# Kernel optimization log

Hardware: AMD Instinct MI355X
Metric: run time of the kernel (lower is better)

The kernel has to match this reference:

```python
import jax, jax.numpy as jnp
import numpy as np

N_VERT = 163842  # icosphere level-7 vertex count
IN_FEATS = 64
OUT_FEATS = 64
BATCH = 2
K = 7  # center vertex + 6 one-ring neighbors


def setup_inputs() -> dict:
    key = jax.random.key(0)
    k1, k2, k3, k4 = jax.random.split(key, 4)
    x = jax.random.normal(k1, (N_VERT, IN_FEATS, BATCH), dtype=jnp.float32)
    neigh_orders = jax.random.randint(k2, (K * N_VERT,), 0, N_VERT, dtype=jnp.int64)
    W = jax.random.normal(k3, (OUT_FEATS, K * IN_FEATS), dtype=jnp.float32) * 0.05
    b = jax.random.normal(k4, (OUT_FEATS,), dtype=jnp.float32) * 0.05
    return {"x": x, "neigh_orders": neigh_orders, "W": W, "b": b}


def reference(x, neigh_orders, W, b):
    # x: [N, C, B]; neigh_orders: [7N] flat indices, grouped per-vertex (n*7 + k)
    N = x.shape[0]
    C = x.shape[1]
    idx = neigh_orders.reshape(N, K)            # [N, 7]
    gathered = x[idx]                           # [N, 7, C, B] irregular gather
    Wr = W.reshape(W.shape[0], K, C)            # [O, 7, C] matches flatten order (k*C + c)
    # out[n, o, b] = sum_{k,c} gathered[n,k,c,b] * W[o, k*C + c] + b[o]
    out = jnp.einsum("nkcb,okc->nob", gathered, Wr) + b[None, :, None]
    return out  # [N, O, B]
```

## Files before the change

kernel.cpp:

```cpp
#include <hip/hip_runtime.h>

#define NV      163842
#define CIN     64
#define KN      7
#define NKMAX   (NV * KN)
#define KDIM    448
#define KSTEPS  14
#define VPC     16
#define ROWS    32
#define ASTRIDE 456

typedef short  short8 __attribute__((ext_vector_type(8)));
typedef float  f32x4  __attribute__((ext_vector_type(4)));

static __device__ __forceinline__ unsigned int pack_bf16(float a, float b) {
#if __has_builtin(__builtin_amdgcn_cvt_pk_bf16_f32)
    typedef __bf16 bf16x2 __attribute__((ext_vector_type(2)));
    union { bf16x2 v; unsigned int u; } cv;
    cv.v = __builtin_amdgcn_cvt_pk_bf16_f32(a, b);
    return cv.u;
#else
    unsigned int ua = __float_as_uint(a);
    unsigned int ub = __float_as_uint(b);
    ua = (ua + 0x7FFFu + ((ua >> 16) & 1u)) >> 16;
    ub = (ub + 0x7FFFu + ((ub >> 16) & 1u)) & 0xFFFF0000u;
    return ua | ub;
#endif
}

static __device__ __forceinline__ void bar_lgkm() {
    asm volatile("s_waitcnt lgkmcnt(0)\n\ts_barrier" ::: "memory");
}

__global__ __launch_bounds__(256)
void xcast(const float* __restrict__ x, unsigned int* __restrict__ xt, int nf4)
{
    const int f = blockIdx.x * 256 + threadIdx.x;
    if (f >= nf4) return;
    const f32x4 g = __builtin_nontemporal_load(&((const f32x4*)x)[f]);
    const int v = f >> 5;
    const int r = f & 31;
    xt[v * 32 + r]           = pack_bf16(g[0], g[2]);
    xt[NV * 32 + v * 32 + r] = pack_bf16(g[1], g[3]);
}

__global__ __launch_bounds__(256, 3)
void onering_mfma_bf16(const unsigned short* __restrict__ xt,
                       const int* __restrict__ neigh,
                       const float* __restrict__ W,
                       const float* __restrict__ bias,
                       float* __restrict__ out,
                       int nchunks)
{
    __shared__ unsigned short A_lds[ROWS * ASTRIDE];
    __shared__ float          C_lds[VPC * 128];

    const int tid  = threadIdx.x;
    const int lane = tid & 63;
    const int w    = tid >> 6;
    const int ncol = lane & 15;
    const int kgrp = lane >> 4;
    const int G    = gridDim.x;

    short8 bfrag[KSTEPS];
    {
        const int o = w * 16 + ncol;
#pragma unroll
        for (int s = 0; s < KSTEPS; ++s) {
            const int kb = s * 32 + kgrp * 8;
            const float4* wp = (const float4*)(W + o * KDIM + kb);
            float4 w0 = wp[0];
            float4 w1 = wp[1];
            union { short8 v; unsigned int u[4]; } pk;
            pk.u[0] = pack_bf16(w0.x, w0.y);
            pk.u[1] = pack_bf16(w0.z, w0.w);
            pk.u[2] = pack_bf16(w1.x, w1.y);
            pk.u[3] = pack_bf16(w1.z, w1.w);
            bfrag[s] = pk.v;
        }
    }
    const float biasv = bias[w * 16 + ncol];

    const int l8 = tid & 7;
    int nidx[7];
    int lbyte[7];
    int soff[7];
#pragma unroll
    for (int i = 0; i < 7; ++i) {
        const int seg = (tid >> 3) + 32 * i;
        const int row = seg / 7;
        const int k   = seg - row * 7;
        const int lv  = row >> 1, bb = row & 1;
        nidx[i]  = lv * KN + k;
        lbyte[i] = row * (ASTRIDE * 2) + k * 128 + l8 * 16;
        soff[i]  = bb * (NV * 64) + l8 * 8;
    }

    const int ch0 = blockIdx.x;
    int    I[7];
    short8 R[7];

#pragma unroll
    for (int i = 0; i < 7; ++i) {
        int gi = ch0 * (VPC * KN) + nidx[i];
        I[i] = __builtin_nontemporal_load(&neigh[gi < NKMAX ? gi : 0]);
    }
#pragma unroll
    for (int i = 0; i < 7; ++i)
        R[i] = *(const short8*)(xt + soff[i] + I[i] * 64);
#pragma unroll
    for (int i = 0; i < 7; ++i) {
        int gi = (ch0 + G) * (VPC * KN) + nidx[i];
        I[i] = __builtin_nontemporal_load(&neigh[gi < NKMAX ? gi : 0]);
    }

    for (int ch = ch0; ch < nchunks; ch += G) {
        const int vb = ch * VPC;

        bar_lgkm();

#pragma unroll
        for (int i = 0; i < 7; ++i)
            *(short8*)((char*)A_lds + lbyte[i]) = R[i];
#pragma unroll
        for (int i = 0; i < 7; ++i)
            R[i] = *(const short8*)(xt + soff[i] + I[i] * 64);
#pragma unroll
        for (int i = 0; i < 7; ++i) {
            int gi = (ch + 2 * G) * (VPC * KN) + nidx[i];
            I[i] = __builtin_nontemporal_load(&neigh[gi < NKMAX ? gi : 0]);
        }

        bar_lgkm();

        f32x4 acc0 = {0.f, 0.f, 0.f, 0.f};
        f32x4 acc1 = {0.f, 0.f, 0.f, 0.f};
#pragma unroll
        for (int s = 0; s < KSTEPS; ++s) {
            const int kb = s * 32 + kgrp * 8;
            const short8 a0 = *(const short8*)&A_lds[ncol * ASTRIDE + kb];
            const short8 a1 = *(const short8*)&A_lds[(16 + ncol) * ASTRIDE + kb];
            acc0 = __builtin_amdgcn_mfma_f32_16x16x32_bf16(a0, bfrag[s], acc0, 0, 0, 0);
            acc1 = __builtin_amdgcn_mfma_f32_16x16x32_bf16(a1, bfrag[s], acc1, 0, 0, 0);
        }

        const int o2 = (w * 16 + ncol) * 2;
#pragma unroll
        for (int j = 0; j < 4; ++j) {
            const int r  = kgrp * 4 + j;
            C_lds[(r >> 1) * 128 + o2 + (r & 1)] = acc0[j] + biasv;
            const int r2 = 16 + r;
            C_lds[(r2 >> 1) * 128 + o2 + (r2 & 1)] = acc1[j] + biasv;
        }

        bar_lgkm();

        f32x4* dst = (f32x4*)(out + vb * 128);
#pragma unroll
        for (int it = 0; it < 2; ++it) {
            const int fidx = tid + 256 * it;
            if (vb + (fidx >> 5) < NV)
                __builtin_nontemporal_store(((const f32x4*)C_lds)[fidx], &dst[fidx]);
        }
    }
}

__global__ __launch_bounds__(256, 4)
void onering_mfma_f32(const float* __restrict__ x,
                      const int* __restrict__ neigh,
                      const float* __restrict__ W,
                      const float* __restrict__ bias,
                      float* __restrict__ out,
                      int nchunks)
{
    __shared__ unsigned short A_lds[ROWS * ASTRIDE];
    const int tid  = threadIdx.x;
    const int lane = tid & 63;
    const int w    = tid >> 6;
    const int ncol = lane & 15;
    const int kgrp = lane >> 4;

    short8 bfrag[KSTEPS];
    {
        const int o = w * 16 + ncol;
#pragma unroll
        for (int s = 0; s < KSTEPS; ++s) {
            const int kb = s * 32 + kgrp * 8;
            const float4* wp = (const float4*)(W + o * KDIM + kb);
            float4 w0 = wp[0];
            float4 w1 = wp[1];
            union { short8 v; unsigned int u[4]; } pk;
            pk.u[0] = pack_bf16(w0.x, w0.y);
            pk.u[1] = pack_bf16(w0.z, w0.w);
            pk.u[2] = pack_bf16(w1.x, w1.y);
            pk.u[3] = pack_bf16(w1.z, w1.w);
            bfrag[s] = pk.v;
        }
    }
    const float biasv = bias[w * 16 + ncol];
    const int off4  = tid & 31;
    const int sbase = tid >> 5;

    for (int ch = blockIdx.x; ch < nchunks; ch += gridDim.x) {
        const int vb = ch * VPC;
        __syncthreads();
#pragma unroll
        for (int i = 0; i < 14; ++i) {
            const int s  = sbase + 8 * i;
            const int lv = s / 7;
            const int k  = s - lv * 7;
            const int n  = vb + lv;
            int vi = 0;
            if (n < NV) vi = neigh[n * KN + k];
            const float4 g = ((const float4*)x)[vi * 32 + off4];
            const int base = k * 64 + 2 * off4;
            ((unsigned int*)A_lds)[((lv * 2)     * ASTRIDE + base) >> 1] = pack_bf16(g.x, g.z);
            ((unsigned int*)A_lds)[((lv * 2 + 1) * ASTRIDE + base) >> 1] = pack_bf16(g.y, g.w);
        }
        __syncthreads();
        f32x4 acc0 = {0.f, 0.f, 0.f, 0.f};
        f32x4 acc1 = {0.f, 0.f, 0.f, 0.f};
#pragma unroll
        for (int s = 0; s < KSTEPS; ++s) {
            const int kb = s * 32 + kgrp * 8;
            const short8 a0 = *(const short8*)&A_lds[ncol * ASTRIDE + kb];
            const short8 a1 = *(const short8*)&A_lds[(16 + ncol) * ASTRIDE + kb];
            acc0 = __builtin_amdgcn_mfma_f32_16x16x32_bf16(a0, bfrag[s], acc0, 0, 0, 0);
            acc1 = __builtin_amdgcn_mfma_f32_16x16x32_bf16(a1, bfrag[s], acc1, 0, 0, 0);
        }
        const int o = w * 16 + ncol;
#pragma unroll
        for (int j = 0; j < 4; ++j) {
            const int r = kgrp * 4 + j;
            {
                const int lv = r >> 1, bb = r & 1, n = vb + lv;
                if (n < NV) out[n * 128 + o * 2 + bb] = acc0[j] + biasv;
            }
            {
                const int m = 16 + r;
                const int lv = m >> 1, bb = m & 1, n = vb + lv;
                if (n < NV) out[n * 128 + o * 2 + bb] = acc1[j] + biasv;
            }
        }
    }
}

extern "C" void kernel_launch(void* const* d_in, const int* in_sizes, int n_in,
                              void* d_out, int out_size, void* d_ws, size_t ws_size,
                              hipStream_t stream) {
    const float* x     = (const float*)d_in[0];
    const int*   neigh = (const int*)d_in[1];
    const float* W     = (const float*)d_in[2];
    const float* bias  = (const float*)d_in[3];
    float*       out   = (float*)d_out;

    const int nchunks = (NV + VPC - 1) / VPC;
    const size_t need = (size_t)2 * NV * 64 * sizeof(unsigned short);

    if (ws_size >= need) {
        unsigned short* xt = (unsigned short*)d_ws;
        const int nf4 = NV * 32;
        xcast<<<dim3((nf4 + 255) / 256), dim3(256), 0, stream>>>(x, (unsigned int*)xt, nf4);
        onering_mfma_bf16<<<dim3(2560), dim3(256), 0, stream>>>(xt, neigh, W, bias, out, nchunks);
    } else {
        onering_mfma_f32<<<dim3(2560), dim3(256), 0, stream>>>(x, neigh, W, bias, out, nchunks);
    }
}
```

Baseline: 212.6 us.

## Load gathered A-fragments straight into registers and drop LDS staging

The bf16 kernel now has each lane gather its MFMA A-operand fragments directly from global memory into registers, skipping the LDS tile, the barriers and the LDS output staging. Work is re-split so each wave handles 8 vertices × 2 batches against 32 output features, using two B fragments per k-step. Gathers for the next chunk are issued in the MFMA loop, and results are written straight to global with 8-byte nontemporal stores. The intent is to cut LDS traffic and barrier stalls. The cost is more VGPRs (occupancy hint lowered to 2, grid cut to 2048), smaller scattered stores, and weights held twice per wave.

After: 284.6 us. 1.34x slower.

```diff
diff --git a/kernel.cpp b/kernel.cpp
--- a/kernel.cpp
+++ b/kernel.cpp
@@ -7,11 +7,10 @@
 #define KDIM    448
 #define KSTEPS  14
 #define VPC     16
-#define ROWS    32
-#define ASTRIDE 456
 
 typedef short  short8 __attribute__((ext_vector_type(8)));
 typedef float  f32x4  __attribute__((ext_vector_type(4)));
+typedef float  f32x2  __attribute__((ext_vector_type(2)));
 
 static __device__ __forceinline__ unsigned int pack_bf16(float a, float b) {
 #if __has_builtin(__builtin_amdgcn_cvt_pk_bf16_f32)
@@ -28,10 +27,6 @@
 #endif
 }
 
-static __device__ __forceinline__ void bar_lgkm() {
-    asm volatile("s_waitcnt lgkmcnt(0)\n\ts_barrier" ::: "memory");
-}
-
 __global__ __launch_bounds__(256)
 void xcast(const float* __restrict__ x, unsigned int* __restrict__ xt, int nf4)
 {
@@ -44,7 +39,7 @@
     xt[NV * 32 + v * 32 + r] = pack_bf16(g[1], g[3]);
 }
 
-__global__ __launch_bounds__(256, 3)
+__global__ __launch_bounds__(256, 2)
 void onering_mfma_bf16(const unsigned short* __restrict__ xt,
                        const int* __restrict__ neigh,
                        const float* __restrict__ W,
@@ -52,21 +47,21 @@
                        float* __restrict__ out,
                        int nchunks)
 {
-    __shared__ unsigned short A_lds[ROWS * ASTRIDE];
-    __shared__ float          C_lds[VPC * 128];
-
     const int tid  = threadIdx.x;
     const int lane = tid & 63;
     const int w    = tid >> 6;
+    const int mt   = w & 1;
+    const int oh   = w >> 1;
     const int ncol = lane & 15;
     const int kgrp = lane >> 4;
     const int G    = gridDim.x;
 
-    short8 bfrag[KSTEPS];
-    {
-        const int o = w * 16 + ncol;
-#pragma unroll
-        for (int s = 0; s < KSTEPS; ++s) {
+    short8 bfrag[KSTEPS][2];
+#pragma unroll
+    for (int s = 0; s < KSTEPS; ++s) {
+#pragma unroll
+        for (int ot = 0; ot < 2; ++ot) {
+            const int o  = oh * 32 + ot * 16 + ncol;
             const int kb = s * 32 + kgrp * 8;
             const float4* wp = (const float4*)(W + o * KDIM + kb);
             float4 w0 = wp[0];
@@ -76,95 +71,76 @@
             pk.u[1] = pack_bf16(w0.z, w0.w);
             pk.u[2] = pack_bf16(w1.x, w1.y);
             pk.u[3] = pack_bf16(w1.z, w1.w);
-            bfrag[s] = pk.v;
-        }
-    }
-    const float biasv = bias[w * 16 + ncol];
-
-    const int l8 = tid & 7;
-    int nidx[7];
-    int lbyte[7];
-    int soff[7];
-#pragma unroll
-    for (int i = 0; i < 7; ++i) {
-        const int seg = (tid >> 3) + 32 * i;
-        const int row = seg / 7;
-        const int k   = seg - row * 7;
-        const int lv  = row >> 1, bb = row & 1;
-        nidx[i]  = lv * KN + k;
-        lbyte[i] = row * (ASTRIDE * 2) + k * 128 + l8 * 16;
-        soff[i]  = bb * (NV * 64) + l8 * 8;
-    }
+            bfrag[s][ot] = pk.v;
+        }
+    }
+    const float bias0 = bias[oh * 32 + ncol];
+    const float bias1 = bias[oh * 32 + 16 + ncol];
+
+    const int lv  = mt * 8 + (ncol >> 1);
+    const int bb  = ncol & 1;
+    const unsigned short* xtb = xt + (size_t)bb * (NV * 64);
+    const int nbase = lv * KN;
 
     const int ch0 = blockIdx.x;
-    int    I[7];
-    short8 R[7];
-
-#pragma unroll
-    for (int i = 0; i < 7; ++i) {
-        int gi = ch0 * (VPC * KN) + nidx[i];
-        I[i] = __builtin_nontemporal_load(&neigh[gi < NKMAX ? gi : 0]);
-    }
-#pragma unroll
-    for (int i = 0; i < 7; ++i)
-        R[i] = *(const short8*)(xt + soff[i] + I[i] * 64);
-#pragma unroll
-    for (int i = 0; i < 7; ++i) {
-        int gi = (ch0 + G) * (VPC * KN) + nidx[i];
-        I[i] = __builtin_nontemporal_load(&neigh[gi < NKMAX ? gi : 0]);
+    short8 R[KSTEPS];
+    int    I[KN];
+
+    {
+        int Ic[KN];
+#pragma unroll
+        for (int k2 = 0; k2 < KN; ++k2) {
+            int gi = ch0 * (VPC * KN) + nbase + k2;
+            Ic[k2] = __builtin_nontemporal_load(&neigh[gi < NKMAX ? gi : 0]);
+        }
+#pragma unroll
+        for (int s = 0; s < KSTEPS; ++s) {
+            const int c0 = (s & 1) * 32 + kgrp * 8;
+            R[s] = *(const short8*)(xtb + Ic[s >> 1] * 64 + c0);
+        }
+#pragma unroll
+        for (int k2 = 0; k2 < KN; ++k2) {
+            int gi = (ch0 + G) * (VPC * KN) + nbase + k2;
+            I[k2] = __builtin_nontemporal_load(&neigh[gi < NKMAX ? gi : 0]);
+        }
     }
 
     for (int ch = ch0; ch < nchunks; ch += G) {
         const int vb = ch * VPC;
 
-        bar_lgkm();
-
-#pragma unroll
-        for (int i = 0; i < 7; ++i)
-            *(short8*)((char*)A_lds + lbyte[i]) = R[i];
-#pragma unroll
-        for (int i = 0; i < 7; ++i)
-            R[i] = *(const short8*)(xt + soff[i] + I[i] * 64);
-#pragma unroll
-        for (int i = 0; i < 7; ++i) {
-            int gi = (ch + 2 * G) * (VPC * KN) + nidx[i];
-            I[i] = __builtin_nontemporal_load(&neigh[gi < NKMAX ? gi : 0]);
-        }
-
-        bar_lgkm();
-
         f32x4 acc0 = {0.f, 0.f, 0.f, 0.f};
         f32x4 acc1 = {0.f, 0.f, 0.f, 0.f};
 #pragma unroll
         for (int s = 0; s < KSTEPS; ++s) {
-            const int kb = s * 32 + kgrp * 8;
-            const short8 a0 = *(const short8*)&A_lds[ncol * ASTRIDE + kb];
-            const short8 a1 = *(const short8*)&A_lds[(16 + ncol) * ASTRIDE + kb];
-            acc0 = __builtin_amdgcn_mfma_f32_16x16x32_bf16(a0, bfrag[s], acc0, 0, 0, 0);
-            acc1 = __builtin_amdgcn_mfma_f32_16x16x32_bf16(a1, bfrag[s], acc1, 0, 0, 0);
-        }
-
-        const int o2 = (w * 16 + ncol) * 2;
-#pragma unroll
-        for (int j = 0; j < 4; ++j) {
-            const int r  = kgrp * 4 + j;
-            C_lds[(r >> 1) * 128 + o2 + (r & 1)] = acc0[j] + biasv;
-            const int r2 = 16 + r;
-            C_lds[(r2 >> 1) * 128 + o2 + (r2 & 1)] = acc1[j] + biasv;
-        }
-
-        bar_lgkm();
-
-        f32x4* dst = (f32x4*)(out + vb * 128);
-#pragma unroll
-        for (int it = 0; it < 2; ++it) {
-            const int fidx = tid + 256 * it;
-            if (vb + (fidx >> 5) < NV)
-                __builtin_nontemporal_store(((const f32x4*)C_lds)[fidx], &dst[fidx]);
-        }
-    }
-}
-
+            const short8 a = R[s];
+            acc0 = __builtin_amdgcn_mfma_f32_16x16x32_bf16(a, bfrag[s][0], acc0, 0, 0, 0);
+            acc1 = __builtin_amdgcn_mfma_f32_16x16x32_bf16(a, bfrag[s][1], acc1, 0, 0, 0);
+            const int c0 = (s & 1) * 32 + kgrp * 8;
+            R[s] = *(const short8*)(xtb + I[s >> 1] * 64 + c0);
+        }
+
+#pragma unroll
+        for (int k2 = 0; k2 < KN; ++k2) {
+            int gi = (ch + 2 * G) * (VPC * KN) + nbase + k2;
+            I[k2] = __builtin_nontemporal_load(&neigh[gi < NKMAX ? gi : 0]);
+        }
+
+#pragma unroll
+        for (int jp = 0; jp < 2; ++jp) {
+            const int n = vb + mt * 8 + kgrp * 2 + jp;
+            if (n < NV) {
+                const int o0 = oh * 32 + ncol;
+                f32x2 v0 = {acc0[2 * jp] + bias0, acc0[2 * jp + 1] + bias0};
+                f32x2 v1 = {acc1[2 * jp] + bias1, acc1[2 * jp + 1] + bias1};
+                __builtin_nontemporal_store(v0, (f32x2*)(out + n * 128 + o0 * 2));
+                __builtin_nontemporal_store(v1, (f32x2*)(out + n * 128 + (o0 + 16) * 2));
+            }
+        }
+    }
+}
+
+#define ROWS    32
+#define ASTRIDE 456
 __global__ __launch_bounds__(256, 4)
 void onering_mfma_f32(const float* __restrict__ x,
                       const int* __restrict__ neigh,
@@ -233,13 +209,13 @@
         for (int j = 0; j < 4; ++j) {
             const int r = kgrp * 4 + j;
             {
-                const int lv = r >> 1, bb = r & 1, n = vb + lv;
-                if (n < NV) out[n * 128 + o * 2 + bb] = acc0[j] + biasv;
+                const int lv = r >> 1, b2 = r & 1, n = vb + lv;
+                if (n < NV) out[n * 128 + o * 2 + b2] = acc0[j] + biasv;
             }
             {
                 const int m = 16 + r;
-                const int lv = m >> 1, bb = m & 1, n = vb + lv;
-                if (n < NV) out[n * 128 + o * 2 + bb] = acc1[j] + biasv;
+                const int lv = m >> 1, b2 = m & 1, n = vb + lv;
+                if (n < NV) out[n * 128 + o * 2 + b2] = acc1[j] + biasv;
             }
         }
     }
@@ -261,7 +237,7 @@
         unsigned short* xt = (unsigned short*)d_ws;
         const int nf4 = NV * 32;
         xcast<<<dim3((nf4 + 255) / 256), dim3(256), 0, stream>>>(x, (unsigned int*)xt, nf4);
-        onering_mfma_bf16<<<dim3(2560), dim3(256), 0, stream>>>(xt, neigh, W, bias, out, nchunks);
+        onering_mfma_bf16<<<dim3(2048), dim3(256), 0, stream>>>(xt, neigh, W, bias, out, nchunks);
     } else {
         onering_mfma_f32<<<dim3(2560), dim3(256), 0, stream>>>(x, neigh, W, bias, out, nchunks);
     }
```
